# Performance work log

Hardware: AMD Instinct MI355X
Metric: run time of the kernel (lower is better)

## Reference

```python
import jax, jax.numpy as jnp
import numpy as np

N = 4096
IN_F = 256
OUT_F = 64
K = 4
ALPHA = 0.2  # LeakyReLU negative slope
NEG_INF = -9e15


def setup_inputs() -> dict:
    key = jax.random.key(0)
    k_h, k_w, k_a, k_e, k_m = jax.random.split(key, 5)
    h = jax.random.normal(k_h, (N, IN_F), dtype=jnp.float32)
    # xavier_uniform with gain=1.414
    def xavier(k, shape, gain=1.414):
        fan_in, fan_out = shape[0], shape[1]
        limit = gain * np.sqrt(6.0 / (fan_in + fan_out))
        return jax.random.uniform(k, shape, jnp.float32, -limit, limit)
    W = xavier(k_w, (IN_F, OUT_F))
    a = xavier(k_a, (2 * OUT_F, 1))
    vals = jax.random.uniform(k_e, (K, N, N), dtype=jnp.float32)
    mask = jax.random.uniform(k_m, (K, N, N), dtype=jnp.float32) < 0.05
    edge_attr = jnp.where(mask, vals, 0.0)
    return {"h": h, "edge_attr": edge_attr, "W": W, "a": a}


def reference(h, edge_attr, W, a):
    # h: [N, IN_F], edge_attr: [K, N, N], W: [IN_F, OUT_F], a: [2*OUT_F, 1]
    Wh = h @ W                                   # [N, OUT_F]
    Wh1 = Wh @ a[:OUT_F, :]                      # [N, 1]
    Wh2 = Wh @ a[OUT_F:, :]                      # [N, 1]
    e = jax.nn.leaky_relu(Wh1 + Wh2.T, negative_slope=ALPHA)  # [N, N]
    e = e[None, :, :] * edge_attr                # [K, N, N]
    e = jnp.where(edge_attr > 0, e, NEG_INF)
    att = jax.nn.softmax(e, axis=1)              # softmax over dim=1, as in torch
    # dropout is identity in eval mode
    # batched replacement for the per-channel python loop of matmuls
    hp = jnp.einsum('kij,jf->kif', att, Wh)      # [K, N, OUT_F]
    out = jnp.transpose(hp, (1, 0, 2)).reshape(N, K * OUT_F)  # concat dim=1
    return jax.nn.elu(out), att
```

## Files before the change

kernel.cpp:

```cpp
#include <hip/hip_runtime.h>

#define NN 4096
#define IN_F 256
#define OUT_F 64
#define K_CH 4
#define ALPHA 0.2f
#define JP 8
#define JCOLS 512
#define ROWS1 16
#define IC1 256

typedef __bf16 bf16;
typedef __attribute__((ext_vector_type(8))) __bf16 bf16x8;
typedef __attribute__((ext_vector_type(4))) float f32x4;

__global__ __launch_bounds__(256) void k0_wh(const float* __restrict__ h,
                                             const float* __restrict__ W,
                                             const float* __restrict__ a,
                                             float* __restrict__ Wh,
                                             float* __restrict__ Wh1,
                                             float* __restrict__ Wh2) {
    int tid = threadIdx.x;
    int wave = tid >> 6, lane = tid & 63;
    int i = blockIdx.x * 4 + wave;
    const float* hrow = h + (size_t)i * IN_F;
    float acc = 0.f;
    #pragma unroll 8
    for (int c = 0; c < IN_F; ++c)
        acc += hrow[c] * W[c * OUT_F + lane];
    Wh[(size_t)i * OUT_F + lane] = acc;
    float v1 = acc * a[lane];
    float v2 = acc * a[OUT_F + lane];
    #pragma unroll
    for (int o = 32; o > 0; o >>= 1) {
        v1 += __shfl_xor(v1, o, 64);
        v2 += __shfl_xor(v2, o, 64);
    }
    if (lane == 0) { Wh1[i] = v1; Wh2[i] = v2; }
}

__global__ __launch_bounds__(256) void k0_transpose(const float* __restrict__ Wh,
                                                    bf16* __restrict__ WhT) {
    __shared__ float lds[OUT_F * 65];
    int tid = threadIdx.x;
    int i0 = blockIdx.x * 64;
    int f = tid & 63;
    int r0 = tid >> 6;
    #pragma unroll
    for (int s = 0; s < 16; ++s) {
        int r = r0 * 16 + s;
        lds[f * 65 + r] = Wh[(size_t)(i0 + r) * OUT_F + f];
    }
    __syncthreads();
    int f2 = tid >> 2;
    int c0 = (tid & 3) * 16;
    #pragma unroll
    for (int s = 0; s < 16; ++s) {
        int c = c0 + s;
        WhT[(size_t)f2 * NN + i0 + c] = (bf16)lds[f2 * 65 + c];
    }
}

__global__ __launch_bounds__(256) void k1_colsum(const float* __restrict__ edge_ch,
                                                 const float* __restrict__ Wh1,
                                                 const float* __restrict__ Wh2,
                                                 bf16* __restrict__ p_ch,
                                                 float* __restrict__ partial) {
    int tid = threadIdx.x;
    int j0 = blockIdx.y * 2048 + tid * 8;
    int ic = blockIdx.x;
    int ibase = ic * ROWS1;
    float w2[8];
    {
        f32x4 t0 = *(const f32x4*)&Wh2[j0];
        f32x4 t1 = *(const f32x4*)&Wh2[j0 + 4];
        #pragma unroll
        for (int c = 0; c < 4; ++c) { w2[c] = t0[c]; w2[c + 4] = t1[c]; }
    }
    float s[8] = {0.f, 0.f, 0.f, 0.f, 0.f, 0.f, 0.f, 0.f};
    const float* base = edge_ch + (size_t)ibase * NN + j0;
    bf16* pbase = p_ch + (size_t)ibase * NN + j0;
    f32x4 r0[4], r1[4];
    #pragma unroll
    for (int t = 0; t < 4; ++t) {
        r0[t] = *(const f32x4*)(base + (size_t)t * NN);
        r1[t] = *(const f32x4*)(base + (size_t)t * NN + 4);
    }
    #pragma unroll 4
    for (int ii = 0; ii < ROWS1; ++ii) {
        int cur = ii & 3;
        f32x4 e0 = r0[cur], e1 = r1[cur];
        int ip = (ii + 4 < ROWS1) ? ii + 4 : ii;
        r0[cur] = *(const f32x4*)(base + (size_t)ip * NN);
        r1[cur] = *(const f32x4*)(base + (size_t)ip * NN + 4);
        float wh1 = Wh1[ibase + ii];
        bf16x8 pv;
        #pragma unroll
        for (int c = 0; c < 8; ++c) {
            float ef = c < 4 ? e0[c] : e1[c - 4];
            float xv = wh1 + w2[c];
            float lk = xv > 0.f ? xv : ALPHA * xv;
            float val = ef > 0.f ? __expf(lk * ef) : 0.f;
            bf16 vb = (bf16)val;
            pv[c] = vb;
            s[c] += (float)vb;
        }
        *(bf16x8*)(pbase + (size_t)ii * NN) = pv;
    }
    float* pr = partial + (size_t)ic * NN + j0;
    f32x4 o0, o1;
    #pragma unroll
    for (int c = 0; c < 4; ++c) { o0[c] = s[c]; o1[c] = s[c + 4]; }
    *(f32x4*)pr = o0;
    *(f32x4*)(pr + 4) = o1;
}

__global__ __launch_bounds__(256) void k1_reduce(const float* __restrict__ partial,
                                                 float* __restrict__ s_col) {
    __shared__ float red[256];
    int tid = threadIdx.x;
    int jl = tid & 63, g = tid >> 6;
    int j = blockIdx.x * 64 + jl;
    float s = 0.f;
    #pragma unroll 8
    for (int t = 0; t < IC1 / 4; ++t)
        s += partial[(size_t)(g * (IC1 / 4) + t) * NN + j];
    red[tid] = s;
    __syncthreads();
    if (tid < 64)
        s_col[j] = red[tid] + red[tid + 64] + red[tid + 128] + red[tid + 192];
}

__global__ __launch_bounds__(256) void k2_fused(const bf16* __restrict__ p_ch,
                                                const float* __restrict__ s_col,
                                                const bf16* __restrict__ WhT,
                                                float* __restrict__ att_ch,
                                                float* __restrict__ hp) {
    __shared__ float lds_inv[JCOLS];
    int tid = threadIdx.x;
    int itile = blockIdx.x;
    int jp = blockIdx.y;
    int jbase0 = jp * JCOLS;
    {
        int t2 = tid * 2;
        float s0 = s_col[jbase0 + t2];
        float s1 = s_col[jbase0 + t2 + 1];
        lds_inv[t2]     = s0 > 0.f ? 1.f / s0 : 0.f;
        lds_inv[t2 + 1] = s1 > 0.f ? 1.f / s1 : 0.f;
    }
    __syncthreads();
    int wave = tid >> 6, lane = tid & 63;
    int n16 = lane & 15, quad = lane >> 4;
    int i_row = itile * 64 + wave * 16 + n16;
    const size_t ebase = (size_t)i_row * NN + jbase0 + quad * 8;
    const bf16* pptr = p_ch + ebase;
    float* aptr = att_ch + ebase;
    const bf16* wbase = WhT + (size_t)n16 * NN + jbase0 + quad * 8;
    f32x4 acc[4] = {};
    bf16x8 pf[4];
    #pragma unroll
    for (int t = 0; t < 4; ++t)
        pf[t] = *(const bf16x8*)(pptr + t * 32);
    #pragma unroll 4
    for (int s = 0; s < JCOLS / 32; ++s) {
        int cur = s & 3;
        bf16x8 pv = pf[cur];
        int sp = (s + 4 < JCOLS / 32) ? s + 4 : s;
        pf[cur] = *(const bf16x8*)(pptr + sp * 32);
        int jl = s * 32 + quad * 8;
        f32x4 iv0 = *(const f32x4*)&lds_inv[jl];
        f32x4 iv1 = *(const f32x4*)&lds_inv[jl + 4];
        bf16x8 afrag;
        f32x4 av0, av1;
        #pragma unroll
        for (int c = 0; c < 8; ++c) {
            float isc = c < 4 ? iv0[c] : iv1[c - 4];
            float attv = (float)pv[c] * isc;
            afrag[c] = (bf16)attv;
            if (c < 4) av0[c] = attv; else av1[c - 4] = attv;
        }
        __builtin_nontemporal_store(av0, (f32x4*)(aptr + s * 32));
        __builtin_nontemporal_store(av1, (f32x4*)(aptr + s * 32 + 4));
        #pragma unroll
        for (int ft = 0; ft < 4; ++ft) {
            bf16x8 bfrag = *(const bf16x8*)(wbase + (size_t)ft * 16 * NN + s * 32);
            acc[ft] = __builtin_amdgcn_mfma_f32_16x16x32_bf16(afrag, bfrag, acc[ft], 0, 0, 0);
        }
    }
    #pragma unroll
    for (int ft = 0; ft < 4; ++ft) {
        #pragma unroll
        for (int r = 0; r < 4; ++r) {
            int row_l = quad * 4 + r;
            int i_g = itile * 64 + wave * 16 + row_l;
            size_t idx = ((size_t)jp * NN + i_g) * OUT_F + ft * 16 + n16;
            hp[idx] = acc[ft][r];
        }
    }
}

__global__ __launch_bounds__(256) void k3_combine(const float* __restrict__ hp,
                                                  float* __restrict__ out,
                                                  int kch) {
    int g = blockIdx.x * 256 + threadIdx.x;
    int i = g >> 6;
    int f = g & 63;
    float s = 0.f;
    #pragma unroll
    for (int z = 0; z < JP; ++z)
        s += hp[((size_t)z * NN + i) * OUT_F + f];
    out[(size_t)i * (K_CH * OUT_F) + kch * OUT_F + f] = s > 0.f ? s : __expf(s) - 1.f;
}

extern "C" void kernel_launch(void* const* d_in, const int* in_sizes, int n_in,
                              void* d_out, int out_size, void* d_ws, size_t ws_size,
                              hipStream_t stream) {
    (void)out_size; (void)ws_size;
    const float *h = nullptr, *edge = nullptr, *W = nullptr, *a = nullptr;
    for (int i = 0; i < n_in; ++i) {
        int sz = in_sizes[i];
        if (sz == NN * IN_F)               h    = (const float*)d_in[i];
        else if (sz == K_CH * NN * NN)     edge = (const float*)d_in[i];
        else if (sz == IN_F * OUT_F)       W    = (const float*)d_in[i];
        else if (sz == 2 * OUT_F)          a    = (const float*)d_in[i];
    }

    char* ws = (char*)d_ws;
    size_t off = 0;
    float* Wh      = (float*)(ws + off); off += (size_t)NN * OUT_F * 4;
    float* Wh1     = (float*)(ws + off); off += NN * 4;
    float* Wh2     = (float*)(ws + off); off += NN * 4;
    float* s_col   = (float*)(ws + off); off += NN * 4;
    bf16*  WhT     = (bf16*) (ws + off); off += (size_t)OUT_F * NN * 2;
    float* partial = (float*)(ws + off); off += (size_t)IC1 * NN * 4;
    float* hp      = (float*)(ws + off); off += (size_t)JP * NN * OUT_F * 4;
    bf16*  p_buf   = (bf16*) (ws + off); off += (size_t)NN * NN * 2;

    float* out_h   = (float*)d_out;
    float* att_out = out_h + (size_t)NN * (K_CH * OUT_F);

    k0_wh<<<dim3(NN / 4), 256, 0, stream>>>(h, W, a, Wh, Wh1, Wh2);
    k0_transpose<<<dim3(NN / 64), 256, 0, stream>>>(Wh, WhT);

    for (int ch = 0; ch < K_CH; ++ch) {
        const float* edge_ch = edge + (size_t)ch * NN * NN;
        float* att_ch = att_out + (size_t)ch * NN * NN;
        k1_colsum<<<dim3(IC1, 2), 256, 0, stream>>>(edge_ch, Wh1, Wh2, p_buf, partial);
        k1_reduce<<<dim3(NN / 64), 256, 0, stream>>>(partial, s_col);
        k2_fused<<<dim3(64, JP), 256, 0, stream>>>(p_buf, s_col, WhT, att_ch, hp);
        k3_combine<<<dim3(NN * OUT_F / 256), 256, 0, stream>>>(hp, out_h, ch);
    }
}
```

Before: 644.6 us.

## Batch all channels into single launches per stage instead of per-channel loop

After: 625.2 us. -3.0%, faster.

```diff
diff --git a/kernel.cpp b/kernel.cpp
--- a/kernel.cpp
+++ b/kernel.cpp
@@ -61,12 +61,13 @@
     }
 }
 
-__global__ __launch_bounds__(256) void k1_colsum(const float* __restrict__ edge_ch,
+__global__ __launch_bounds__(256) void k1_colsum(const float* __restrict__ edge,
                                                  const float* __restrict__ Wh1,
                                                  const float* __restrict__ Wh2,
-                                                 bf16* __restrict__ p_ch,
+                                                 bf16* __restrict__ p_buf,
                                                  float* __restrict__ partial) {
     int tid = threadIdx.x;
+    int kch = blockIdx.z;
     int j0 = blockIdx.y * 2048 + tid * 8;
     int ic = blockIdx.x;
     int ibase = ic * ROWS1;
@@ -78,8 +79,8 @@
         for (int c = 0; c < 4; ++c) { w2[c] = t0[c]; w2[c + 4] = t1[c]; }
     }
     float s[8] = {0.f, 0.f, 0.f, 0.f, 0.f, 0.f, 0.f, 0.f};
-    const float* base = edge_ch + (size_t)ibase * NN + j0;
-    bf16* pbase = p_ch + (size_t)ibase * NN + j0;
+    const float* base = edge + ((size_t)kch * NN + ibase) * NN + j0;
+    bf16* pbase = p_buf + ((size_t)kch * NN + ibase) * NN + j0;
     f32x4 r0[4], r1[4];
     #pragma unroll
     for (int t = 0; t < 4; ++t) {
@@ -107,7 +108,7 @@
         }
         *(bf16x8*)(pbase + (size_t)ii * NN) = pv;
     }
-    float* pr = partial + (size_t)ic * NN + j0;
+    float* pr = partial + ((size_t)kch * IC1 + ic) * NN + j0;
     f32x4 o0, o1;
     #pragma unroll
     for (int c = 0; c < 4; ++c) { o0[c] = s[c]; o1[c] = s[c + 4]; }
@@ -116,45 +117,48 @@
 }
 
 __global__ __launch_bounds__(256) void k1_reduce(const float* __restrict__ partial,
-                                                 float* __restrict__ s_col) {
+                                                 float* __restrict__ s_inv) {
     __shared__ float red[256];
     int tid = threadIdx.x;
+    int kch = blockIdx.y;
     int jl = tid & 63, g = tid >> 6;
     int j = blockIdx.x * 64 + jl;
+    const float* pb = partial + (size_t)kch * IC1 * NN;
     float s = 0.f;
     #pragma unroll 8
     for (int t = 0; t < IC1 / 4; ++t)
-        s += partial[(size_t)(g * (IC1 / 4) + t) * NN + j];
+        s += pb[(size_t)(g * (IC1 / 4) + t) * NN + j];
     red[tid] = s;
     __syncthreads();
-    if (tid < 64)
-        s_col[j] = red[tid] + red[tid + 64] + red[tid + 128] + red[tid + 192];
-}
-
-__global__ __launch_bounds__(256) void k2_fused(const bf16* __restrict__ p_ch,
-                                                const float* __restrict__ s_col,
+    if (tid < 64) {
+        float tot = red[tid] + red[tid + 64] + red[tid + 128] + red[tid + 192];
+        s_inv[kch * NN + j] = tot > 0.f ? 1.f / tot : 0.f;
+    }
+}
+
+__global__ __launch_bounds__(256) void k2_fused(const bf16* __restrict__ p_buf,
+                                                const float* __restrict__ s_inv,
                                                 const bf16* __restrict__ WhT,
-                                                float* __restrict__ att_ch,
+                                                float* __restrict__ att_out,
                                                 float* __restrict__ hp) {
     __shared__ float lds_inv[JCOLS];
     int tid = threadIdx.x;
     int itile = blockIdx.x;
-    int jp = blockIdx.y;
+    int z = blockIdx.y;
+    int kch = z >> 3, jp = z & 7;
     int jbase0 = jp * JCOLS;
     {
         int t2 = tid * 2;
-        float s0 = s_col[jbase0 + t2];
-        float s1 = s_col[jbase0 + t2 + 1];
-        lds_inv[t2]     = s0 > 0.f ? 1.f / s0 : 0.f;
-        lds_inv[t2 + 1] = s1 > 0.f ? 1.f / s1 : 0.f;
+        lds_inv[t2]     = s_inv[kch * NN + jbase0 + t2];
+        lds_inv[t2 + 1] = s_inv[kch * NN + jbase0 + t2 + 1];
     }
     __syncthreads();
     int wave = tid >> 6, lane = tid & 63;
     int n16 = lane & 15, quad = lane >> 4;
     int i_row = itile * 64 + wave * 16 + n16;
-    const size_t ebase = (size_t)i_row * NN + jbase0 + quad * 8;
-    const bf16* pptr = p_ch + ebase;
-    float* aptr = att_ch + ebase;
+    const size_t ebase = ((size_t)kch * NN + i_row) * NN + jbase0 + quad * 8;
+    const bf16* pptr = p_buf + ebase;
+    float* aptr = att_out + ebase;
     const bf16* wbase = WhT + (size_t)n16 * NN + jbase0 + quad * 8;
     f32x4 acc[4] = {};
     bf16x8 pf[4];
@@ -193,23 +197,24 @@
         for (int r = 0; r < 4; ++r) {
             int row_l = quad * 4 + r;
             int i_g = itile * 64 + wave * 16 + row_l;
-            size_t idx = ((size_t)jp * NN + i_g) * OUT_F + ft * 16 + n16;
+            size_t idx = ((size_t)z * NN + i_g) * OUT_F + ft * 16 + n16;
             hp[idx] = acc[ft][r];
         }
     }
 }
 
 __global__ __launch_bounds__(256) void k3_combine(const float* __restrict__ hp,
-                                                  float* __restrict__ out,
-                                                  int kch) {
+                                                  float* __restrict__ out) {
     int g = blockIdx.x * 256 + threadIdx.x;
-    int i = g >> 6;
-    int f = g & 63;
+    int i = g >> 8;
+    int rem = g & 255;
+    int kch = rem >> 6;
+    int f = rem & 63;
     float s = 0.f;
     #pragma unroll
     for (int z = 0; z < JP; ++z)
-        s += hp[((size_t)z * NN + i) * OUT_F + f];
-    out[(size_t)i * (K_CH * OUT_F) + kch * OUT_F + f] = s > 0.f ? s : __expf(s) - 1.f;
+        s += hp[(((size_t)(kch * JP + z)) * NN + i) * OUT_F + f];
+    out[g] = s > 0.f ? s : __expf(s) - 1.f;
 }
 
 extern "C" void kernel_launch(void* const* d_in, const int* in_sizes, int n_in,
@@ -230,24 +235,19 @@
     float* Wh      = (float*)(ws + off); off += (size_t)NN * OUT_F * 4;
     float* Wh1     = (float*)(ws + off); off += NN * 4;
     float* Wh2     = (float*)(ws + off); off += NN * 4;
-    float* s_col   = (float*)(ws + off); off += NN * 4;
+    float* s_inv   = (float*)(ws + off); off += (size_t)K_CH * NN * 4;
     bf16*  WhT     = (bf16*) (ws + off); off += (size_t)OUT_F * NN * 2;
-    float* partial = (float*)(ws + off); off += (size_t)IC1 * NN * 4;
-    float* hp      = (float*)(ws + off); off += (size_t)JP * NN * OUT_F * 4;
-    bf16*  p_buf   = (bf16*) (ws + off); off += (size_t)NN * NN * 2;
+    float* partial = (float*)(ws + off); off += (size_t)K_CH * IC1 * NN * 4;
+    float* hp      = (float*)(ws + off); off += (size_t)K_CH * JP * NN * OUT_F * 4;
+    bf16*  p_buf   = (bf16*) (ws + off); off += (size_t)K_CH * NN * NN * 2;
 
     float* out_h   = (float*)d_out;
     float* att_out = out_h + (size_t)NN * (K_CH * OUT_F);
 
     k0_wh<<<dim3(NN / 4), 256, 0, stream>>>(h, W, a, Wh, Wh1, Wh2);
     k0_transpose<<<dim3(NN / 64), 256, 0, stream>>>(Wh, WhT);
-
-    for (int ch = 0; ch < K_CH; ++ch) {
-        const float* edge_ch = edge + (size_t)ch * NN * NN;
-        float* att_ch = att_out + (size_t)ch * NN * NN;
-        k1_colsum<<<dim3(IC1, 2), 256, 0, stream>>>(edge_ch, Wh1, Wh2, p_buf, partial);
-        k1_reduce<<<dim3(NN / 64), 256, 0, stream>>>(partial, s_col);
-        k2_fused<<<dim3(64, JP), 256, 0, stream>>>(p_buf, s_col, WhT, att_ch, hp);
-        k3_combine<<<dim3(NN * OUT_F / 256), 256, 0, stream>>>(hp, out_h, ch);
-    }
-}
+    k1_colsum<<<dim3(IC1, 2, K_CH), 256, 0, stream>>>(edge, Wh1, Wh2, p_buf, partial);
+    k1_reduce<<<dim3(NN / 64, K_CH), 256, 0, stream>>>(partial, s_inv);
+    k2_fused<<<dim3(64, K_CH * JP), 256, 0, stream>>>(p_buf, s_inv, WhT, att_out, hp);
+    k3_combine<<<dim3((NN * K_CH * OUT_F) / 256), 256, 0, stream>>>(hp, out_h);
+}
```
